# Optimization experiments

Hardware: AMD Instinct MI355X
Metric: run time of the kernel (lower is better)

## Reference

```python
import jax, jax.numpy as jnp
import numpy as np

NB, NG = 131072, 32768            # n_bus, n_gen nodes
EBB, EGB, EBG = 2097152, 65536, 65536  # bus-bus, gen->bus, bus->gen edges
CIN, C, COUT = 32, 64, 32         # in_channels, n_channels, out_channels
NL, NT = 2, 5                     # n_layers, n_taps+1
EPS = 1e-5


def setup_inputs() -> dict:
    key = jax.random.key(0)
    ks = iter(jax.random.split(key, 40))
    rn = lambda shape, s=1.0: jax.random.normal(next(ks), shape, dtype=jnp.float32) * s
    ri = lambda shape, hi: jax.random.randint(next(ks), shape, 0, hi, dtype=jnp.int32)
    inp = {
        'x_bus': rn((NB, CIN)), 'x_gen': rn((NG, CIN)),
        'readin_W_bus': rn((CIN, C), CIN ** -0.5), 'readin_b_bus': jnp.zeros((C,), jnp.float32),
        'readin_W_gen': rn((CIN, C), CIN ** -0.5), 'readin_b_gen': jnp.zeros((C,), jnp.float32),
        'bn_gamma_bus': jnp.ones((NL, C), jnp.float32), 'bn_beta_bus': jnp.zeros((NL, C), jnp.float32),
        'bn_gamma_gen': jnp.ones((NL, C), jnp.float32), 'bn_beta_gen': jnp.zeros((NL, C), jnp.float32),
        'taps_W_bus': rn((NL, NT, C, C), C ** -0.5), 'taps_b_bus': jnp.zeros((NL, NT, C), jnp.float32),
        'taps_W_gen': rn((NL, NT, C, C), C ** -0.5), 'taps_b_gen': jnp.zeros((NL, NT, C), jnp.float32),
        'readout_W_bus': rn((C, COUT), C ** -0.5), 'readout_b_bus': jnp.zeros((COUT,), jnp.float32),
        'readout_W_gen': rn((C, COUT), C ** -0.5), 'readout_b_gen': jnp.zeros((COUT,), jnp.float32),
        'edge_bb': ri((2, EBB), NB),
        'edge_gb_src': ri((EGB,), NG), 'edge_gb_dst': ri((EGB,), NB),
        'edge_bg_src': ri((EBG,), NB), 'edge_bg_dst': ri((EBG,), NG),
    }
    return inp


def _lrelu(v):
    return jnp.where(v >= 0, v, 0.01 * v)  # nn.LeakyReLU default slope


def _bn(v, g, b):
    # training-mode BatchNorm over the node dimension (biased variance)
    m = jnp.mean(v, axis=0)
    s = jnp.var(v, axis=0)
    return (v - m) * jax.lax.rsqrt(s + EPS) * g + b


def reference(x_bus, x_gen,
              readin_W_bus, readin_b_bus, readin_W_gen, readin_b_gen,
              bn_gamma_bus, bn_beta_bus, bn_gamma_gen, bn_beta_gen,
              taps_W_bus, taps_b_bus, taps_W_gen, taps_b_gen,
              readout_W_bus, readout_b_bus, readout_W_gen, readout_b_gen,
              edge_bb, edge_gb_src, edge_gb_dst, edge_bg_src, edge_bg_dst):
    seg = jax.ops.segment_sum
    bbs, bbd = edge_bb[0], edge_bb[1]
    # readin (single HeteroDictLinear, plain_last)
    xb = x_bus @ readin_W_bus + readin_b_bus   # [NB, C]
    xg = x_gen @ readin_W_gen + readin_b_gen   # [NG, C]
    for l in range(NL):  # residual blocks: norm -> act -> (dropout p=0) -> graph filter -> +x
        yb = _lrelu(_bn(xb, bn_gamma_bus[l], bn_beta_bus[l]))
        yg = _lrelu(_bn(xg, bn_gamma_gen[l], bn_beta_gen[l]))
        zb = yb @ taps_W_bus[l, 0] + taps_b_bus[l, 0]
        zg = yg @ taps_W_gen[l, 0] + taps_b_gen[l, 0]
        cb, cg = yb, yg
        for k in range(1, NT):  # graph shift (scatter-add over hetero edges) + per-type tap
            nb = seg(cb[bbs], bbd, num_segments=NB) + seg(cg[edge_gb_src], edge_gb_dst, num_segments=NB)
            ng = seg(cb[edge_bg_src], edge_bg_dst, num_segments=NG)
            cb, cg = nb, ng
            zb = zb + cb @ taps_W_bus[l, k] + taps_b_bus[l, k]
            zg = zg + cg @ taps_W_gen[l, k] + taps_b_gen[l, k]
        xb = xb + zb
        xg = xg + zg
    out_b = xb @ readout_W_bus + readout_b_bus  # [NB, COUT]
    out_g = xg @ readout_W_gen + readout_b_gen  # [NG, COUT]
    return (out_b, out_g)
```

## Files before the change

### kernel.cpp

```cpp
#include <hip/hip_runtime.h>

#define NBUS 131072
#define NGEN 32768
#define NALL (NBUS + NGEN)
#define NEBB 2097152
#define NEGB 65536
#define NEBG 65536
#define NEBUS (NEBB + NEGB)
#define NTILE (NALL / 64)
#define NTILE_BUS (NBUS / 64)
#define NGB 2560

typedef float f32x2 __attribute__((ext_vector_type(2)));
typedef float f32x4 __attribute__((ext_vector_type(4)));
typedef short s16x8 __attribute__((ext_vector_type(8)));
typedef unsigned short u16;

__device__ inline f32x2 bf2x2(unsigned v) {
  f32x2 r;
  r.x = __builtin_bit_cast(float, v << 16);
  r.y = __builtin_bit_cast(float, v & 0xFFFF0000u);
  return r;
}
__device__ inline u16 f2bf(float f) {
  unsigned u = __builtin_bit_cast(unsigned, f);
  unsigned r = u + 0x7FFFu + ((u >> 16) & 1u);
  return (u16)(r >> 16);
}
__device__ inline unsigned pack2bf(float a, float b) {
  return (unsigned)f2bf(a) | ((unsigned)f2bf(b) << 16);
}

__global__ void __launch_bounds__(256) k_convw(const float* __restrict__ tWb,
                                               const float* __restrict__ tWg,
                                               const float* __restrict__ roWb,
                                               const float* __restrict__ roWg,
                                               const float* __restrict__ riWb,
                                               const float* __restrict__ riWg,
                                               u16* __restrict__ wt,
                                               u16* __restrict__ rot,
                                               u16* __restrict__ riwt) {
  int t = blockIdx.x * 256 + threadIdx.x;
  int S = gridDim.x * 256;
  for (int i = t; i < 20 * 4096; i += S) {
    int mat = i >> 12, off = i & 4095, n = off >> 6, k = off & 63;
    const float* src = (mat < 10) ? tWb : tWg;
    int tap = (mat < 10) ? mat : mat - 10;
    wt[i] = f2bf(src[(size_t)tap * 4096 + k * 64 + n]);
  }
  for (int i = t; i < 2 * 2048; i += S) {
    int type = i >> 11, off = i & 2047, n = off >> 6, k = off & 63;
    const float* src = type ? roWg : roWb;
    rot[i] = f2bf(src[k * 32 + n]);
  }
  for (int i = t; i < 2 * 2048; i += S) {
    int type = i >> 11, off = i & 2047, n = off >> 5, k = off & 31;
    const float* src = type ? riWg : riWb;
    riwt[i] = f2bf(src[k * 64 + n]);
  }
}

__device__ inline void dev_hist(int bid, const int* __restrict__ bbDst,
                                const int* __restrict__ gbDst,
                                const int* __restrict__ bgDst,
                                int* __restrict__ busCnt, int* __restrict__ bgCnt) {
  const int g = bid & 7;
  const int blk = bid >> 3;
  const int start = blk * 256 + threadIdx.x;
  const int S = 256 * 256;
  int i = start;
  for (; i + 3 * S < NEBB; i += 4 * S) {
    int d0 = bbDst[i], d1 = bbDst[i + S], d2 = bbDst[i + 2 * S], d3 = bbDst[i + 3 * S];
    if ((d0 >> 14) == g) atomicAdd(&busCnt[d0], 1);
    if ((d1 >> 14) == g) atomicAdd(&busCnt[d1], 1);
    if ((d2 >> 14) == g) atomicAdd(&busCnt[d2], 1);
    if ((d3 >> 14) == g) atomicAdd(&busCnt[d3], 1);
  }
  for (; i < NEBB; i += S) {
    int d = bbDst[i];
    if ((d >> 14) == g) atomicAdd(&busCnt[d], 1);
  }
  for (i = start; i < NEGB; i += S) {
    int d = gbDst[i];
    if ((d >> 14) == g) atomicAdd(&busCnt[d], 1);
  }
  for (i = start; i < NEBG; i += S) {
    int d = bgDst[i];
    if ((d >> 12) == g) atomicAdd(&bgCnt[d], 1);
  }
}

__device__ inline void dev_readin(int tile, const float* __restrict__ xbus,
                                  const float* __restrict__ xgen,
                                  const u16* __restrict__ riwt,
                                  const float* __restrict__ bb_,
                                  const float* __restrict__ bg_,
                                  float* __restrict__ y, float* __restrict__ stats) {
  __shared__ float sst[128];
  const bool isBus = tile < NTILE_BUS;
  const int tid = threadIdx.x, lane = tid & 63, wv = tid >> 6;
  const int m = lane & 15, kq = lane >> 4;
  const int grow = tile * 64 + wv * 16 + m;
  const float* xp = isBus ? &xbus[(size_t)grow * 32] : &xgen[(size_t)(grow - NBUS) * 32];
  s16x8 a;
#pragma unroll
  for (int j = 0; j < 8; j++) a[j] = (short)f2bf(xp[kq * 8 + j]);
  const u16* rb = riwt + (size_t)(isBus ? 0 : 1) * 2048;
  const float* bb = isBus ? bb_ : bg_;
  f32x4 acc[4];
#pragma unroll
  for (int cb = 0; cb < 4; cb++) {
    acc[cb] = (f32x4){0.f, 0.f, 0.f, 0.f};
    const u16* wp = rb + (cb * 16 + m) * 32 + kq * 8;
    s16x8 b = *(const s16x8*)wp;
    acc[cb] = __builtin_amdgcn_mfma_f32_16x16x32_bf16(a, b, acc[cb], 0, 0, 0);
  }
  if (tid < 128) sst[tid] = 0.f;
  __syncthreads();
  const int orow0 = tile * 64 + wv * 16 + kq * 4;
#pragma unroll
  for (int cb = 0; cb < 4; cb++) {
    int col = cb * 16 + m;
    float bv = bb[col];
    float s1 = 0.f, s2 = 0.f;
#pragma unroll
    for (int i = 0; i < 4; i++) {
      float yo = acc[cb][i] + bv;
      y[(size_t)(orow0 + i) * 64 + col] = yo;
      s1 += yo;
      s2 = fmaf(yo, yo, s2);
    }
    atomicAdd(&sst[col], s1);
    atomicAdd(&sst[64 + col], s2);
  }
  __syncthreads();
  if (tid < 64) {
    atomicAdd(&stats[(isBus ? 0 : 128) + tid], sst[tid]);
    atomicAdd(&stats[(isBus ? 0 : 128) + 64 + tid], sst[64 + tid]);
  }
}

__global__ void __launch_bounds__(256) k_hist_readin(
    const int* __restrict__ bbDst, const int* __restrict__ gbDst,
    const int* __restrict__ bgDst, int* __restrict__ busCnt, int* __restrict__ bgCnt,
    const float* __restrict__ xbus, const float* __restrict__ xgen,
    const u16* __restrict__ riwt, const float* __restrict__ bb_,
    const float* __restrict__ bg_, float* __restrict__ y, float* __restrict__ stats) {
  if (blockIdx.x < 2048)
    dev_hist(blockIdx.x, bbDst, gbDst, bgDst, busCnt, bgCnt);
  else
    dev_readin(blockIdx.x - 2048, xbus, xgen, riwt, bb_, bg_, y, stats);
}

__device__ inline void dev_scan1(int bid, const int* __restrict__ in,
                                 int* __restrict__ out, int* __restrict__ bsums, int n) {
  __shared__ int sh[256];
  int t = threadIdx.x;
  int base = bid * 1024 + t * 4;
  int v0 = (base + 0 < n) ? in[base + 0] : 0;
  int v1 = (base + 1 < n) ? in[base + 1] : 0;
  int v2 = (base + 2 < n) ? in[base + 2] : 0;
  int v3 = (base + 3 < n) ? in[base + 3] : 0;
  int t0 = v0, t1 = t0 + v1, t2 = t1 + v2, t3 = t2 + v3;
  sh[t] = t3;
  __syncthreads();
  for (int off = 1; off < 256; off <<= 1) {
    int x = (t >= off) ? sh[t - off] : 0;
    __syncthreads();
    sh[t] += x;
    __syncthreads();
  }
  int excl = (t > 0) ? sh[t - 1] : 0;
  if (base + 0 < n) out[base + 0] = excl;
  if (base + 1 < n) out[base + 1] = excl + t0;
  if (base + 2 < n) out[base + 2] = excl + t1;
  if (base + 3 < n) out[base + 3] = excl + t2;
  if (t == 255) bsums[bid] = sh[255];
}

__global__ void k_scanA(const int* __restrict__ busCnt, int* __restrict__ busOff,
                        int* __restrict__ bsums, const int* __restrict__ bgCnt,
                        int* __restrict__ bgOff, int* __restrict__ bsums2) {
  if (blockIdx.x < 128)
    dev_scan1(blockIdx.x, busCnt, busOff, bsums, NBUS);
  else
    dev_scan1(blockIdx.x - 128, bgCnt, bgOff, bsums2, NGEN);
}

__device__ inline void dev_scan2(int* __restrict__ bsums, int nb) {
  __shared__ int sh[256];
  int t = threadIdx.x;
  int v = (t < nb) ? bsums[t] : 0;
  sh[t] = v;
  __syncthreads();
  for (int off = 1; off < 256; off <<= 1) {
    int x = (t >= off) ? sh[t - off] : 0;
    __syncthreads();
    sh[t] += x;
    __syncthreads();
  }
  int excl = (t > 0) ? sh[t - 1] : 0;
  if (t < nb) bsums[t] = excl;
}

__global__ void k_scanB(int* __restrict__ bsums, int* __restrict__ bsums2) {
  if (blockIdx.x == 0)
    dev_scan2(bsums, 128);
  else
    dev_scan2(bsums2, 32);
}

__device__ inline void dev_scan3(int bid, int nblk, int* __restrict__ off,
                                 int* __restrict__ cur, const int* __restrict__ bsums,
                                 int n, int E) {
  int stride = nblk * 256;
  for (int i = bid * 256 + threadIdx.x; i < n; i += stride) {
    int o = off[i] + bsums[i >> 10];
    off[i] = o;
    cur[i] = o;
  }
  if (bid == 0 && threadIdx.x == 0) off[n] = E;
}

__global__ void k_scanC(int* __restrict__ busOff, int* __restrict__ busCur,
                        const int* __restrict__ bsums, int* __restrict__ bgOff,
                        int* __restrict__ bgCur, const int* __restrict__ bsums2) {
  if (blockIdx.x < 512)
    dev_scan3(blockIdx.x, 512, busOff, busCur, bsums, NBUS, NEBUS);
  else
    dev_scan3(blockIdx.x - 512, 128, bgOff, bgCur, bsums2, NGEN, NEBG);
}

__device__ inline void dev_fill(int bid, const int* __restrict__ bbSrc,
                                const int* __restrict__ bbDst,
                                const int* __restrict__ gbSrc,
                                const int* __restrict__ gbDst,
                                const int* __restrict__ bgSrc,
                                const int* __restrict__ bgDst,
                                int* __restrict__ busCur, int* __restrict__ bgCur,
                                int* __restrict__ busSrt, int* __restrict__ bgSrt) {
  const int g = bid & 7;
  const int tid = threadIdx.x;
  if (bid < 2048) {
    const int blk = bid >> 3;
    const int S = 256 * 256;
    int i = blk * 256 + tid;
    for (; i + 3 * S < NEBB; i += 4 * S) {
      int d0 = bbDst[i], d1 = bbDst[i + S], d2 = bbDst[i + 2 * S], d3 = bbDst[i + 3 * S];
      if ((d0 >> 14) == g) { int p = atomicAdd(&busCur[d0], 1); busSrt[p] = bbSrc[i]; }
      if ((d1 >> 14) == g) { int p = atomicAdd(&busCur[d1], 1); busSrt[p] = bbSrc[i + S]; }
      if ((d2 >> 14) == g) { int p = atomicAdd(&busCur[d2], 1); busSrt[p] = bbSrc[i + 2 * S]; }
      if ((d3 >> 14) == g) { int p = atomicAdd(&busCur[d3], 1); busSrt[p] = bbSrc[i + 3 * S]; }
    }
    for (; i < NEBB; i += S) {
      int d = bbDst[i];
      if ((d >> 14) == g) { int p = atomicAdd(&busCur[d], 1); busSrt[p] = bbSrc[i]; }
    }
  } else if (bid < 2304) {
    const int blk = (bid - 2048) >> 3;
    const int S = 32 * 256;
    for (int i = blk * 256 + tid; i < NEGB; i += S) {
      int d = gbDst[i];
      if ((d >> 14) == g) { int p = atomicAdd(&busCur[d], 1); busSrt[p] = gbSrc[i] + NBUS; }
    }
  } else {
    const int blk = (bid - 2304) >> 3;
    const int S = 32 * 256;
    for (int i = blk * 256 + tid; i < NEBG; i += S) {
      int d = bgDst[i];
      if ((d >> 12) == g) { int p = atomicAdd(&bgCur[d], 1); bgSrt[p] = bgSrc[i]; }
    }
  }
}

__device__ inline void dev_norm(int tile, float* __restrict__ x, u16* __restrict__ c0,
                                const float* __restrict__ stats,
                                const float* __restrict__ gammaB,
                                const float* __restrict__ betaB,
                                const float* __restrict__ gammaG,
                                const float* __restrict__ betaG,
                                const u16* __restrict__ wt,
                                const float* __restrict__ tbb,
                                const float* __restrict__ tbg, int tapIdx) {
  __shared__ u16 yt[64][72];
  const bool isBus = tile < NTILE_BUS;
  const int tid = threadIdx.x, lane = tid & 63, wv = tid >> 6;
  int so = isBus ? 0 : 128;
  float invN = isBus ? (1.0f / NBUS) : (1.0f / NGEN);
  float mn = stats[so + lane] * invN;
  float m2 = stats[so + 64 + lane] * invN;
  float rs = rsqrtf(m2 - mn * mn + 1e-5f);
  float scale = (isBus ? gammaB : gammaG)[lane] * rs;
  float shift = (isBus ? betaB : betaG)[lane] - mn * scale;
  unsigned* cu = (unsigned*)c0;
  int rw0 = tile * 64 + wv * 16;
  for (int i = 0; i < 16; i++) {
    int row = rw0 + i;
    float xv = x[(size_t)row * 64 + lane];
    float y = fmaf(xv, scale, shift);
    y = (y >= 0.f) ? y : 0.01f * y;
    float ypair = __shfl(y, lane ^ 1, 64);
    if ((lane & 1) == 0) {
      unsigned pk = pack2bf(y, ypair);
      cu[(size_t)row * 32 + (lane >> 1)] = pk;
      *(unsigned*)&yt[wv * 16 + i][lane] = pk;
    }
  }
  __syncthreads();
  const int m = lane & 15, kq = lane >> 4;
  const u16* wrow = wt + (size_t)((isBus ? 0 : 10) + tapIdx) * 4096;
  const float* bbase = isBus ? tbb : tbg;
  int lr = wv * 16 + m;
  s16x8 a0 = *(const s16x8*)&yt[lr][kq * 8];
  s16x8 a1 = *(const s16x8*)&yt[lr][32 + kq * 8];
  f32x4 acc[4];
#pragma unroll
  for (int cb = 0; cb < 4; cb++) acc[cb] = (f32x4){0.f, 0.f, 0.f, 0.f};
#pragma unroll
  for (int cb = 0; cb < 4; cb++) {
    const u16* wp = wrow + (cb * 16 + m) * 64 + kq * 8;
    s16x8 b0 = *(const s16x8*)&wp[0];
    s16x8 b1 = *(const s16x8*)&wp[32];
    acc[cb] = __builtin_amdgcn_mfma_f32_16x16x32_bf16(a0, b0, acc[cb], 0, 0, 0);
    acc[cb] = __builtin_amdgcn_mfma_f32_16x16x32_bf16(a1, b1, acc[cb], 0, 0, 0);
  }
  const int orow0 = tile * 64 + wv * 16 + kq * 4;
#pragma unroll
  for (int cb = 0; cb < 4; cb++) {
    int col = cb * 16 + m;
    float bsv = bbase[(size_t)tapIdx * 64 + col];
#pragma unroll
    for (int i = 0; i < 4; i++) {
      size_t idx = (size_t)(orow0 + i) * 64 + col;
      x[idx] += acc[cb][i] + bsv;
    }
  }
}

__global__ void __launch_bounds__(256) k_fill_norm(
    const int* __restrict__ bbSrc, const int* __restrict__ bbDst,
    const int* __restrict__ gbSrc, const int* __restrict__ gbDst,
    const int* __restrict__ bgSrc, const int* __restrict__ bgDst,
    int* __restrict__ busCur, int* __restrict__ bgCur,
    int* __restrict__ busSrt, int* __restrict__ bgSrt,
    float* __restrict__ x, u16* __restrict__ c0, const float* __restrict__ stats,
    const float* __restrict__ gammaB, const float* __restrict__ betaB,
    const float* __restrict__ gammaG, const float* __restrict__ betaG,
    const u16* __restrict__ wt, const float* __restrict__ tbb,
    const float* __restrict__ tbg, int tapIdx) {
  if (blockIdx.x < 2560)
    dev_fill(blockIdx.x, bbSrc, bbDst, gbSrc, gbDst, bgSrc, bgDst,
             busCur, bgCur, busSrt, bgSrt);
  else
    dev_norm(blockIdx.x - 2560, x, c0, stats, gammaB, betaB, gammaG, betaG,
             wt, tbb, tbg, tapIdx);
}

__global__ void __launch_bounds__(256) k_norm(
    float* __restrict__ x, u16* __restrict__ c0, const float* __restrict__ stats,
    const float* __restrict__ gammaB, const float* __restrict__ betaB,
    const float* __restrict__ gammaG, const float* __restrict__ betaG,
    const u16* __restrict__ wt, const float* __restrict__ tbb,
    const float* __restrict__ tbg, int tapIdx) {
  dev_norm(blockIdx.x, x, c0, stats, gammaB, betaB, gammaG, betaG,
           wt, tbb, tbg, tapIdx);
}

__device__ inline void dev_gather(int bid, const int* __restrict__ busOff,
                                  const int* __restrict__ busSrt,
                                  const int* __restrict__ bgOff,
                                  const int* __restrict__ bgSrt,
                                  const u16* __restrict__ src, u16* __restrict__ dst) {
  const int lane = threadIdx.x & 63;
  const int wv = threadIdx.x >> 6;
  const int grp = lane >> 3;
  const int sub = lane & 7;
  const int gb = grp << 3;
  const unsigned* s32 = (const unsigned*)src;
  unsigned* d32 = (unsigned*)dst;
  int rowBase = (bid * 4 + wv) * 8;
  for (int row0 = rowBase; row0 < NALL; row0 += NGB * 32) {
    int row = row0 + grp;
    int beg, end;
    const int* srt;
    if (row < NBUS) {
      beg = busOff[row];
      end = busOff[row + 1];
      srt = busSrt;
    } else {
      beg = bgOff[row - NBUS];
      end = bgOff[row - NBUS + 1];
      srt = bgSrt;
    }
    f32x2 a0 = {0.f, 0.f}, a1 = {0.f, 0.f}, a2 = {0.f, 0.f}, a3 = {0.f, 0.f};
    int last = end - 1;
    for (int e = beg; e < end; e += 8) {
      int ei = e + sub;
      int sv = srt[ei <= last ? ei : last];
      uint4 v[8];
#pragma unroll
      for (int j = 0; j < 8; j++) {
        int s = __shfl(sv, gb + j, 64);
        uint4 vv = *(const uint4*)&s32[(size_t)s * 32 + sub * 4];
        if (e + j > last) { vv.x = 0; vv.y = 0; vv.z = 0; vv.w = 0; }
        v[j] = vv;
      }
#pragma unroll
      for (int j = 0; j < 8; j++) {
        a0 += bf2x2(v[j].x);
        a1 += bf2x2(v[j].y);
        a2 += bf2x2(v[j].z);
        a3 += bf2x2(v[j].w);
      }
    }
    uint4 o;
    o.x = pack2bf(a0.x, a0.y);
    o.y = pack2bf(a1.x, a1.y);
    o.z = pack2bf(a2.x, a2.y);
    o.w = pack2bf(a3.x, a3.y);
    *(uint4*)&d32[(size_t)row * 32 + sub * 4] = o;
  }
}

__global__ void __launch_bounds__(256) k_gather(const int* __restrict__ busOff,
                                                const int* __restrict__ busSrt,
                                                const int* __restrict__ bgOff,
                                                const int* __restrict__ bgSrt,
                                                const u16* __restrict__ src,
                                                u16* __restrict__ dst) {
  dev_gather(blockIdx.x, busOff, busSrt, bgOff, bgSrt, src, dst);
}

__device__ inline void dev_tap2(int tile, const u16* __restrict__ cA,
                                const u16* __restrict__ cB, float* __restrict__ x,
                                const u16* __restrict__ wt,
                                const float* __restrict__ tbb,
                                const float* __restrict__ tbg,
                                int idxA, int idxB, float* __restrict__ stats) {
  __shared__ float sst[128];
  const bool isBus = tile < NTILE_BUS;
  const int row0 = tile * 64;
  const int tid = threadIdx.x, lane = tid & 63, wv = tid >> 6;
  const int m = lane & 15, kq = lane >> 4;
  const int arow = row0 + wv * 16 + m;
  const float* bbase = isBus ? tbb : tbg;
  const u16* wbase = wt + (size_t)(isBus ? 0 : 10) * 4096;
  f32x4 acc[4];
#pragma unroll
  for (int cb = 0; cb < 4; cb++) acc[cb] = (f32x4){0.f, 0.f, 0.f, 0.f};
  const u16* cs[2] = {cA, cB};
  const int idxs[2] = {idxA, idxB};
#pragma unroll
  for (int s = 0; s < 2; s++) {
    const u16* c = cs[s];
    s16x8 a0 = *(const s16x8*)&c[(size_t)arow * 64 + kq * 8];
    s16x8 a1 = *(const s16x8*)&c[(size_t)arow * 64 + 32 + kq * 8];
    const u16* wrow = wbase + (size_t)idxs[s] * 4096;
#pragma unroll
    for (int cb = 0; cb < 4; cb++) {
      const u16* wp = wrow + (cb * 16 + m) * 64 + kq * 8;
      s16x8 b0 = *(const s16x8*)&wp[0];
      s16x8 b1 = *(const s16x8*)&wp[32];
      acc[cb] = __builtin_amdgcn_mfma_f32_16x16x32_bf16(a0, b0, acc[cb], 0, 0, 0);
      acc[cb] = __builtin_amdgcn_mfma_f32_16x16x32_bf16(a1, b1, acc[cb], 0, 0, 0);
    }
  }
  if (stats) {
    if (tid < 128) sst[tid] = 0.f;
    __syncthreads();
  }
  const int orow0 = row0 + wv * 16 + kq * 4;
#pragma unroll
  for (int cb = 0; cb < 4; cb++) {
    int col = cb * 16 + m;
    float bsv = bbase[(size_t)idxA * 64 + col] + bbase[(size_t)idxB * 64 + col];
    float s1 = 0.f, s2 = 0.f;
#pragma unroll
    for (int i = 0; i < 4; i++) {
      size_t idx = (size_t)(orow0 + i) * 64 + col;
      float xo = x[idx] + acc[cb][i] + bsv;
      x[idx] = xo;
      s1 += xo;
      s2 = fmaf(xo, xo, s2);
    }
    if (stats) {
      atomicAdd(&sst[col], s1);
      atomicAdd(&sst[64 + col], s2);
    }
  }
  if (stats) {
    __syncthreads();
    if (tid < 64) {
      atomicAdd(&stats[(isBus ? 0 : 128) + tid], sst[tid]);
      atomicAdd(&stats[(isBus ? 0 : 128) + 64 + tid], sst[64 + tid]);
    }
  }
}

__global__ void __launch_bounds__(256) k_tap2(const u16* __restrict__ cA,
                                              const u16* __restrict__ cB,
                                              float* __restrict__ x,
                                              const u16* __restrict__ wt,
                                              const float* __restrict__ tbb,
                                              const float* __restrict__ tbg,
                                              int idxA, int idxB,
                                              float* __restrict__ stats) {
  dev_tap2(blockIdx.x, cA, cB, x, wt, tbb, tbg, idxA, idxB, stats);
}

__global__ void __launch_bounds__(256) k_gather_tap2(
    const int* __restrict__ busOff, const int* __restrict__ busSrt,
    const int* __restrict__ bgOff, const int* __restrict__ bgSrt,
    const u16* __restrict__ gsrc, u16* __restrict__ gdst,
    const u16* __restrict__ cA, const u16* __restrict__ cB, float* __restrict__ x,
    const u16* __restrict__ wt, const float* __restrict__ tbb,
    const float* __restrict__ tbg, int idxA, int idxB) {
  if (blockIdx.x < NGB)
    dev_gather(blockIdx.x, busOff, busSrt, bgOff, bgSrt, gsrc, gdst);
  else
    dev_tap2(blockIdx.x - NGB, cA, cB, x, wt, tbb, tbg, idxA, idxB, (float*)nullptr);
}

__global__ void __launch_bounds__(256) k_readout(const float* __restrict__ x,
                                                 const u16* __restrict__ rot,
                                                 const float* __restrict__ robb,
                                                 const float* __restrict__ robg,
                                                 float* __restrict__ out) {
  const int tile = blockIdx.x;
  const bool isBus = tile < NTILE_BUS;
  const int tid = threadIdx.x, lane = tid & 63, wv = tid >> 6;
  const int m = lane & 15, kq = lane >> 4;
  const int arow = tile * 64 + wv * 16 + m;
  const float* xp = &x[(size_t)arow * 64 + kq * 8];
  s16x8 a0, a1;
#pragma unroll
  for (int j = 0; j < 8; j++) a0[j] = (short)f2bf(xp[j]);
#pragma unroll
  for (int j = 0; j < 8; j++) a1[j] = (short)f2bf(xp[32 + j]);
  const u16* rbase = rot + (size_t)(isBus ? 0 : 1) * 2048;
  f32x4 acc[2];
  acc[0] = (f32x4){0.f, 0.f, 0.f, 0.f};
  acc[1] = (f32x4){0.f, 0.f, 0.f, 0.f};
#pragma unroll
  for (int cb = 0; cb < 2; cb++) {
    const u16* wp = rbase + (cb * 16 + m) * 64 + kq * 8;
    s16x8 b0 = *(const s16x8*)&wp[0];
    s16x8 b1 = *(const s16x8*)&wp[32];
    acc[cb] = __builtin_amdgcn_mfma_f32_16x16x32_bf16(a0, b0, acc[cb], 0, 0, 0);
    acc[cb] = __builtin_amdgcn_mfma_f32_16x16x32_bf16(a1, b1, acc[cb], 0, 0, 0);
  }
  const float* bb = isBus ? robb : robg;
  const int orow0 = tile * 64 + wv * 16 + kq * 4;
#pragma unroll
  for (int cb = 0; cb < 2; cb++) {
    int col = cb * 16 + m;
    float bv = bb[col];
#pragma unroll
    for (int i = 0; i < 4; i++)
      out[(size_t)(orow0 + i) * 32 + col] = acc[cb][i] + bv;
  }
}

extern "C" void kernel_launch(void* const* d_in, const int* in_sizes, int n_in,
                              void* d_out, int out_size, void* d_ws, size_t ws_size,
                              hipStream_t stream) {
  const float* x_bus = (const float*)d_in[0];
  const float* x_gen = (const float*)d_in[1];
  const float* riWb = (const float*)d_in[2];
  const float* ribb = (const float*)d_in[3];
  const float* riWg = (const float*)d_in[4];
  const float* ribg = (const float*)d_in[5];
  const float* bng_b = (const float*)d_in[6];
  const float* bnb_b = (const float*)d_in[7];
  const float* bng_g = (const float*)d_in[8];
  const float* bnb_g = (const float*)d_in[9];
  const float* tWb = (const float*)d_in[10];
  const float* tbb = (const float*)d_in[11];
  const float* tWg = (const float*)d_in[12];
  const float* tbg = (const float*)d_in[13];
  const float* roWb = (const float*)d_in[14];
  const float* robb = (const float*)d_in[15];
  const float* roWg = (const float*)d_in[16];
  const float* robg = (const float*)d_in[17];
  const int* ebb = (const int*)d_in[18];
  const int* gb_src = (const int*)d_in[19];
  const int* gb_dst = (const int*)d_in[20];
  const int* bg_src = (const int*)d_in[21];
  const int* bg_dst = (const int*)d_in[22];
  const int* bb_src = ebb;
  const int* bb_dst = ebb + NEBB;

  char* p = (char*)d_ws;
  auto take = [&](size_t bytes) -> void* {
    void* r = (void*)p;
    p += (bytes + 255) & ~(size_t)255;
    return r;
  };
  float* x = (float*)take((size_t)NALL * 64 * 4);
  u16* b0 = (u16*)take((size_t)NALL * 64 * 2);
  u16* b1 = (u16*)take((size_t)NALL * 64 * 2);
  u16* b2 = (u16*)take((size_t)NALL * 64 * 2);
  int* bus_off = (int*)take((size_t)(NBUS + 1) * 4);
  int* bus_srt = (int*)take((size_t)NEBUS * 4);
  int* bg_off = (int*)take((size_t)(NGEN + 1) * 4);
  int* bg_srt = (int*)take((size_t)NEBG * 4);
  int* bsums = (int*)take(256 * 4);
  int* bsums2 = (int*)take(256 * 4);
  u16* wt = (u16*)take((size_t)20 * 4096 * 2);
  u16* rot = (u16*)take((size_t)2 * 2048 * 2);
  u16* riwt = (u16*)take((size_t)2 * 2048 * 2);
  int* bus_cur = (int*)take((size_t)NBUS * 4);
  int* bg_cur = (int*)take((size_t)NGEN * 4);
  float* stats0 = (float*)take(256 * 4);
  float* stats1 = (float*)take(256 * 4);
  size_t zlen = (char*)p - (char*)bus_cur;
  if ((size_t)(p - (char*)d_ws) > ws_size) return;

  hipMemsetAsync(bus_cur, 0, zlen, stream);
  k_convw<<<320, 256, 0, stream>>>(tWb, tWg, roWb, roWg, riWb, riWg, wt, rot, riwt);

  k_hist_readin<<<4608, 256, 0, stream>>>(bb_dst, gb_dst, bg_dst, bus_cur, bg_cur,
                                          x_bus, x_gen, riwt, ribb, ribg, x, stats0);

  k_scanA<<<160, 256, 0, stream>>>(bus_cur, bus_off, bsums, bg_cur, bg_off, bsums2);
  k_scanB<<<2, 256, 0, stream>>>(bsums, bsums2);
  k_scanC<<<640, 256, 0, stream>>>(bus_off, bus_cur, bsums, bg_off, bg_cur, bsums2);

  k_fill_norm<<<5120, 256, 0, stream>>>(bb_src, bb_dst, gb_src, gb_dst, bg_src, bg_dst,
                                        bus_cur, bg_cur, bus_srt, bg_srt,
                                        x, b0, stats0, bng_b, bnb_b, bng_g, bnb_g,
                                        wt, tbb, tbg, 0);

  for (int l = 0; l < 2; l++) {
    if (l == 1)
      k_norm<<<NTILE, 256, 0, stream>>>(x, b0, stats1, bng_b + 64, bnb_b + 64,
                                        bng_g + 64, bnb_g + 64, wt, tbb, tbg, 5);
    k_gather<<<NGB, 256, 0, stream>>>(bus_off, bus_srt, bg_off, bg_srt, b0, b1);
    k_gather<<<NGB, 256, 0, stream>>>(bus_off, bus_srt, bg_off, bg_srt, b1, b2);
    k_gather_tap2<<<NGB + NTILE, 256, 0, stream>>>(bus_off, bus_srt, bg_off, bg_srt,
                                                   b2, b0, b1, b2, x, wt, tbb, tbg,
                                                   l * 5 + 1, l * 5 + 2);
    k_gather<<<NGB, 256, 0, stream>>>(bus_off, bus_srt, bg_off, bg_srt, b0, b1);
    k_tap2<<<NTILE, 256, 0, stream>>>(b0, b1, x, wt, tbb, tbg, l * 5 + 3, l * 5 + 4,
                                      (l == 0) ? stats1 : (float*)nullptr);
  }

  k_readout<<<NTILE, 256, 0, stream>>>(x, rot, robb, robg, (float*)d_out);
}
```

Before: 826.6 us.

## Fuse final tap pair with readout and unroll gather to 16 edges

The last layer's tap2 kernel is merged with the readout GEMM. The updated x tile goes into shared memory as bf16 and is fed straight into the readout MFMA, so x is not written back and reread. Separately, the gather inner loop now handles 16 edges per iteration instead of 8, putting more loads in flight per pass. The cost is higher register pressure in the gather and an extra LDS round trip in the fused kernel.

After: 843.1 us. About the same (+2.0%).

```diff
diff --git a/kernel.cpp b/kernel.cpp
--- a/kernel.cpp
+++ b/kernel.cpp
@@ -394,19 +394,27 @@
     }
     f32x2 a0 = {0.f, 0.f}, a1 = {0.f, 0.f}, a2 = {0.f, 0.f}, a3 = {0.f, 0.f};
     int last = end - 1;
-    for (int e = beg; e < end; e += 8) {
-      int ei = e + sub;
-      int sv = srt[ei <= last ? ei : last];
-      uint4 v[8];
+    for (int e = beg; e < end; e += 16) {
+      int ei0 = e + sub, ei1 = e + 8 + sub;
+      int sv0 = srt[ei0 <= last ? ei0 : last];
+      int sv1 = srt[ei1 <= last ? ei1 : last];
+      uint4 v[16];
 #pragma unroll
       for (int j = 0; j < 8; j++) {
-        int s = __shfl(sv, gb + j, 64);
+        int s = __shfl(sv0, gb + j, 64);
         uint4 vv = *(const uint4*)&s32[(size_t)s * 32 + sub * 4];
         if (e + j > last) { vv.x = 0; vv.y = 0; vv.z = 0; vv.w = 0; }
         v[j] = vv;
       }
 #pragma unroll
       for (int j = 0; j < 8; j++) {
+        int s = __shfl(sv1, gb + j, 64);
+        uint4 vv = *(const uint4*)&s32[(size_t)s * 32 + sub * 4];
+        if (e + 8 + j > last) { vv.x = 0; vv.y = 0; vv.z = 0; vv.w = 0; }
+        v[8 + j] = vv;
+      }
+#pragma unroll
+      for (int j = 0; j < 16; j++) {
         a0 += bf2x2(v[j].x);
         a1 += bf2x2(v[j].y);
         a2 += bf2x2(v[j].z);
@@ -521,43 +529,78 @@
     dev_tap2(blockIdx.x - NGB, cA, cB, x, wt, tbb, tbg, idxA, idxB, (float*)nullptr);
 }
 
-__global__ void __launch_bounds__(256) k_readout(const float* __restrict__ x,
-                                                 const u16* __restrict__ rot,
-                                                 const float* __restrict__ robb,
-                                                 const float* __restrict__ robg,
-                                                 float* __restrict__ out) {
+__global__ void __launch_bounds__(256) k_tap2_ro(
+    const u16* __restrict__ cA, const u16* __restrict__ cB,
+    const float* __restrict__ x, const u16* __restrict__ wt,
+    const float* __restrict__ tbb, const float* __restrict__ tbg,
+    int idxA, int idxB, const u16* __restrict__ rot,
+    const float* __restrict__ robb, const float* __restrict__ robg,
+    float* __restrict__ out) {
+  __shared__ u16 yt[64][72];
   const int tile = blockIdx.x;
   const bool isBus = tile < NTILE_BUS;
+  const int row0 = tile * 64;
   const int tid = threadIdx.x, lane = tid & 63, wv = tid >> 6;
   const int m = lane & 15, kq = lane >> 4;
-  const int arow = tile * 64 + wv * 16 + m;
-  const float* xp = &x[(size_t)arow * 64 + kq * 8];
-  s16x8 a0, a1;
-#pragma unroll
-  for (int j = 0; j < 8; j++) a0[j] = (short)f2bf(xp[j]);
-#pragma unroll
-  for (int j = 0; j < 8; j++) a1[j] = (short)f2bf(xp[32 + j]);
+  const int arow = row0 + wv * 16 + m;
+  const float* bbase = isBus ? tbb : tbg;
+  const u16* wbase = wt + (size_t)(isBus ? 0 : 10) * 4096;
+  f32x4 acc[4];
+#pragma unroll
+  for (int cb = 0; cb < 4; cb++) acc[cb] = (f32x4){0.f, 0.f, 0.f, 0.f};
+  const u16* cs[2] = {cA, cB};
+  const int idxs[2] = {idxA, idxB};
+#pragma unroll
+  for (int s = 0; s < 2; s++) {
+    const u16* c = cs[s];
+    s16x8 a0 = *(const s16x8*)&c[(size_t)arow * 64 + kq * 8];
+    s16x8 a1 = *(const s16x8*)&c[(size_t)arow * 64 + 32 + kq * 8];
+    const u16* wrow = wbase + (size_t)idxs[s] * 4096;
+#pragma unroll
+    for (int cb = 0; cb < 4; cb++) {
+      const u16* wp = wrow + (cb * 16 + m) * 64 + kq * 8;
+      s16x8 b0 = *(const s16x8*)&wp[0];
+      s16x8 b1 = *(const s16x8*)&wp[32];
+      acc[cb] = __builtin_amdgcn_mfma_f32_16x16x32_bf16(a0, b0, acc[cb], 0, 0, 0);
+      acc[cb] = __builtin_amdgcn_mfma_f32_16x16x32_bf16(a1, b1, acc[cb], 0, 0, 0);
+    }
+  }
+  const int lrow0 = wv * 16 + kq * 4;
+#pragma unroll
+  for (int cb = 0; cb < 4; cb++) {
+    int col = cb * 16 + m;
+    float bsv = bbase[(size_t)idxA * 64 + col] + bbase[(size_t)idxB * 64 + col];
+#pragma unroll
+    for (int i = 0; i < 4; i++) {
+      float xo = x[(size_t)(row0 + lrow0 + i) * 64 + col] + acc[cb][i] + bsv;
+      yt[lrow0 + i][col] = f2bf(xo);
+    }
+  }
+  __syncthreads();
+  int lr = wv * 16 + m;
+  s16x8 a0 = *(const s16x8*)&yt[lr][kq * 8];
+  s16x8 a1 = *(const s16x8*)&yt[lr][32 + kq * 8];
   const u16* rbase = rot + (size_t)(isBus ? 0 : 1) * 2048;
-  f32x4 acc[2];
-  acc[0] = (f32x4){0.f, 0.f, 0.f, 0.f};
-  acc[1] = (f32x4){0.f, 0.f, 0.f, 0.f};
+  f32x4 racc[2];
+  racc[0] = (f32x4){0.f, 0.f, 0.f, 0.f};
+  racc[1] = (f32x4){0.f, 0.f, 0.f, 0.f};
 #pragma unroll
   for (int cb = 0; cb < 2; cb++) {
     const u16* wp = rbase + (cb * 16 + m) * 64 + kq * 8;
     s16x8 b0 = *(const s16x8*)&wp[0];
     s16x8 b1 = *(const s16x8*)&wp[32];
-    acc[cb] = __builtin_amdgcn_mfma_f32_16x16x32_bf16(a0, b0, acc[cb], 0, 0, 0);
-    acc[cb] = __builtin_amdgcn_mfma_f32_16x16x32_bf16(a1, b1, acc[cb], 0, 0, 0);
+    racc[cb] = __builtin_amdgcn_mfma_f32_16x16x32_bf16(a0, b0, racc[cb], 0, 0, 0);
+    racc[cb] = __builtin_amdgcn_mfma_f32_16x16x32_bf16(a1, b1, racc[cb], 0, 0, 0);
   }
   const float* bb = isBus ? robb : robg;
-  const int orow0 = tile * 64 + wv * 16 + kq * 4;
+  const int orow0 = row0 + wv * 16 + kq * 4;
 #pragma unroll
   for (int cb = 0; cb < 2; cb++) {
     int col = cb * 16 + m;
     float bv = bb[col];
 #pragma unroll
     for (int i = 0; i < 4; i++)
-      out[(size_t)(orow0 + i) * 32 + col] = acc[cb][i] + bv;
+      out[(size_t)(orow0 + i) * 32 + col] = racc[cb][i] + bv;
   }
 }
 
@@ -631,19 +674,20 @@
                                         x, b0, stats0, bng_b, bnb_b, bng_g, bnb_g,
                                         wt, tbb, tbg, 0);
 
-  for (int l = 0; l < 2; l++) {
-    if (l == 1)
-      k_norm<<<NTILE, 256, 0, stream>>>(x, b0, stats1, bng_b + 64, bnb_b + 64,
-                                        bng_g + 64, bnb_g + 64, wt, tbb, tbg, 5);
-    k_gather<<<NGB, 256, 0, stream>>>(bus_off, bus_srt, bg_off, bg_srt, b0, b1);
-    k_gather<<<NGB, 256, 0, stream>>>(bus_off, bus_srt, bg_off, bg_srt, b1, b2);
-    k_gather_tap2<<<NGB + NTILE, 256, 0, stream>>>(bus_off, bus_srt, bg_off, bg_srt,
-                                                   b2, b0, b1, b2, x, wt, tbb, tbg,
-                                                   l * 5 + 1, l * 5 + 2);
-    k_gather<<<NGB, 256, 0, stream>>>(bus_off, bus_srt, bg_off, bg_srt, b0, b1);
-    k_tap2<<<NTILE, 256, 0, stream>>>(b0, b1, x, wt, tbb, tbg, l * 5 + 3, l * 5 + 4,
-                                      (l == 0) ? stats1 : (float*)nullptr);
-  }
-
-  k_readout<<<NTILE, 256, 0, stream>>>(x, rot, robb, robg, (float*)d_out);
-}
+  k_gather<<<NGB, 256, 0, stream>>>(bus_off, bus_srt, bg_off, bg_srt, b0, b1);
+  k_gather<<<NGB, 256, 0, stream>>>(bus_off, bus_srt, bg_off, bg_srt, b1, b2);
+  k_gather_tap2<<<NGB + NTILE, 256, 0, stream>>>(bus_off, bus_srt, bg_off, bg_srt,
+                                                 b2, b0, b1, b2, x, wt, tbb, tbg, 1, 2);
+  k_gather<<<NGB, 256, 0, stream>>>(bus_off, bus_srt, bg_off, bg_srt, b0, b1);
+  k_tap2<<<NTILE, 256, 0, stream>>>(b0, b1, x, wt, tbb, tbg, 3, 4, stats1);
+
+  k_norm<<<NTILE, 256, 0, stream>>>(x, b0, stats1, bng_b + 64, bnb_b + 64,
+                                    bng_g + 64, bnb_g + 64, wt, tbb, tbg, 5);
+  k_gather<<<NGB, 256, 0, stream>>>(bus_off, bus_srt, bg_off, bg_srt, b0, b1);
+  k_gather<<<NGB, 256, 0, stream>>>(bus_off, bus_srt, bg_off, bg_srt, b1, b2);
+  k_gather_tap2<<<NGB + NTILE, 256, 0, stream>>>(bus_off, bus_srt, bg_off, bg_srt,
+                                                 b2, b0, b1, b2, x, wt, tbb, tbg, 6, 7);
+  k_gather<<<NGB, 256, 0, stream>>>(bus_off, bus_srt, bg_off, bg_srt, b0, b1);
+  k_tap2_ro<<<NTILE, 256, 0, stream>>>(b0, b1, x, wt, tbb, tbg, 8, 9,
+                                       rot, robb, robg, (float*)d_out);
+}
```
